# Kernel tuning notes

Hardware: AMD Instinct MI355X
Metric: run time of the kernel (lower is better)

The kernel has to match this reference:

```python
import jax, jax.numpy as jnp
import numpy as np

TEMPERATURE = 0.5
TAU_PLUS = 0.1
EPS = 1e-8


def setup_inputs() -> dict:
    key = jax.random.key(0)
    k1, k2 = jax.random.split(key)
    B, D = 8192, 128
    z_i = jax.random.normal(k1, (B, D), dtype=jnp.float32)
    z_j = jax.random.normal(k2, (B, D), dtype=jnp.float32)
    return {"z_i": z_i, "z_j": z_j}


def _l2_normalize(x, axis=1, eps=1e-12):
    # matches torch F.normalize: x / max(||x||, eps)
    n = jnp.linalg.norm(x, axis=axis, keepdims=True)
    return x / jnp.maximum(n, eps)


def reference(z_i, z_j):
    B = z_i.shape[0]
    zi = _l2_normalize(z_i, axis=1)
    zj = _l2_normalize(z_j, axis=1)
    reps = jnp.concatenate([zi, zj], axis=0)  # [2B, D]
    sim = jnp.matmul(reps, reps.T) / TEMPERATURE  # [2B, 2B]
    sim = sim - jnp.max(sim, axis=1, keepdims=True)
    mask = jnp.eye(2 * B, dtype=bool)
    sim = jnp.where(mask, -9e15, sim)
    pos = jnp.exp(jnp.sum(zi * zj, axis=-1) / TEMPERATURE)  # [B]
    positives = jnp.concatenate([pos, pos], axis=0)  # [2B]
    neg_sum = jnp.sum(jnp.exp(sim), axis=1)  # [2B]
    Ng = (-TAU_PLUS * B * positives + neg_sum) / (1.0 - TAU_PLUS)
    Ng = jnp.maximum(Ng, B * jnp.exp(jnp.asarray(-1.0 / TEMPERATURE, dtype=sim.dtype)))
    loss = -jnp.log(positives / (positives + Ng + EPS))
    return jnp.mean(loss)
```

## Files before the change

### kernel.cpp

```cpp
#include <hip/hip_runtime.h>
#include <hip/hip_bf16.h>

typedef __attribute__((ext_vector_type(8))) short bf16x8;
typedef __attribute__((ext_vector_type(4))) float f32x4;
typedef __attribute__((ext_vector_type(2))) float f32x2;

#define B_ROWS 8192
#define NROWS 16384
#define D 128
#define C1 2.8853900817779268f
#define E_M2 0.13533528323661270f
#define RSCALE 1.6986436f
#define TILE_COLS 32
#define TILE_BYTES (TILE_COLS * D * 2)
#define NSPLIT 16
#define NBLK (64 * NSPLIT)
#define NSLICE 8

__device__ __forceinline__ float fast_exp2(float x) {
#if __has_builtin(__builtin_amdgcn_exp2f)
    return __builtin_amdgcn_exp2f(x);
#else
    float r; asm("v_exp_f32 %0, %1" : "=v"(r) : "v"(x)); return r;
#endif
}
__device__ __forceinline__ float fast_log2(float x) {
#if __has_builtin(__builtin_amdgcn_logf)
    return __builtin_amdgcn_logf(x);
#else
    float r; asm("v_log_f32 %0, %1" : "=v"(r) : "v"(x)); return r;
#endif
}

__device__ __forceinline__ unsigned short f2bf(float f) {
    union { float f; unsigned u; } v; v.f = f;
    unsigned r = v.u + 0x7FFFu + ((v.u >> 16) & 1u);
    return (unsigned short)(r >> 16);
}

__device__ __host__ __forceinline__ int colpart_off(int I) {
    return I * NROWS - 128 * I * (I + 1);
}

__global__ __launch_bounds__(256) void k_norm(const float* __restrict__ zi,
                                              const float* __restrict__ zj,
                                              unsigned* __restrict__ repsU,
                                              float* __restrict__ pos) {
    int w = threadIdx.x >> 6, lane = threadIdx.x & 63;
    int row = blockIdx.x * 4 + w;
    const float2* a2 = (const float2*)(zi + (size_t)row * D);
    const float2* b2 = (const float2*)(zj + (size_t)row * D);
    float2 a = a2[lane], b = b2[lane];
    float si = a.x * a.x + a.y * a.y;
    float sj = b.x * b.x + b.y * b.y;
    float sd = a.x * b.x + a.y * b.y;
#pragma unroll
    for (int m = 32; m; m >>= 1) {
        si += __shfl_xor(si, m);
        sj += __shfl_xor(sj, m);
        sd += __shfl_xor(sd, m);
    }
    float inv_i = 1.0f / fmaxf(sqrtf(si), 1e-12f);
    float inv_j = 1.0f / fmaxf(sqrtf(sj), 1e-12f);
    float sa = inv_i * RSCALE, sb = inv_j * RSCALE;
    repsU[(size_t)row * 64 + lane] =
        (unsigned)f2bf(a.x * sa) | ((unsigned)f2bf(a.y * sa) << 16);
    repsU[(size_t)(row + B_ROWS) * 64 + lane] =
        (unsigned)f2bf(b.x * sb) | ((unsigned)f2bf(b.y * sb) << 16);
    if (lane == 0) pos[row] = fast_exp2(sd * inv_i * inv_j * C1);
}

__global__ __launch_bounds__(256, 2) void k_negsum(const unsigned short* __restrict__ R,
                                                   float* __restrict__ rowpart,
                                                   float* __restrict__ colpart) {
    __shared__ char smem[2][TILE_BYTES];
    __shared__ float colacc[2][16][16][2];
    int I = blockIdx.x >> 4;
    int s = blockIdx.x & (NSPLIT - 1);
    int rowBase = I << 8;
    int j0 = I << 3;
    int dph = (s - (j0 & 15)) & 15;
    int jstart = j0 + dph;
    int nt = (jstart < 512) ? (((511 - jstart) >> 4) + 1) : 0;

    int w = threadIdx.x >> 6;
    int lane = threadIdx.x & 63;
    int lr = lane & 15, lk = lane >> 4;
    int waveRow = rowBase + (w << 6);

    bf16x8 afrag[4][4];
#pragma unroll
    for (int r = 0; r < 4; ++r)
#pragma unroll
        for (int kk = 0; kk < 4; ++kk)
            afrag[r][kk] = *(const bf16x8*)(R + (size_t)(waveRow + r * 16 + lr) * D + kk * 32 + lk * 8);

    int srcoff[2], dstoff[2];
#pragma unroll
    for (int j = 0; j < 2; ++j) {
        int o = (w * 2 + j) * 1024 + lane * 16;
        int row = o >> 8, c = o & 255;
        srcoff[j] = row * 256 + (c ^ ((row & 7) << 4));
        dstoff[j] = (w * 2 + j) * 1024;
    }

    const char* Rb = (const char*)R;

    int m64 = (lr & 4) << 4;
    int lbase = lr * 256 + ((lk * 16) ^ ((lr & 3) << 4));

    float acc[4][4] = {};

#define STAGE(buf, jj)                                                            \
    do {                                                                          \
        const char* tb_ = Rb + (size_t)(jj) * TILE_BYTES;                         \
        _Pragma("unroll")                                                         \
        for (int j = 0; j < 2; ++j)                                               \
            __builtin_amdgcn_global_load_lds(                                     \
                (const __attribute__((address_space(1))) unsigned*)(tb_ + srcoff[j]), \
                (__attribute__((address_space(3))) unsigned*)(&smem[buf][dstoff[j]]), \
                16, 0, 0);                                                        \
    } while (0)

#define BATCH_BODY(DIAG)                                                          \
    do {                                                                          \
        _Pragma("unroll")                                                         \
        for (int ct = 0; ct < 2; ++ct) {                                          \
            const char* cb_ = sb + ct * 4096;                                     \
            bf16x8 b0 = *(const bf16x8*)(cb_ + (0 ^ m64));                        \
            bf16x8 b1 = *(const bf16x8*)(cb_ + (64 ^ m64));                       \
            bf16x8 b2 = *(const bf16x8*)(cb_ + (128 ^ m64));                      \
            bf16x8 b3 = *(const bf16x8*)(cb_ + (192 ^ m64));                      \
            _Pragma("unroll")                                                     \
            for (int r = 0; r < 4; ++r) {                                         \
                f32x4 c = {0.f, 0.f, 0.f, 0.f};                                   \
                c = __builtin_amdgcn_mfma_f32_16x16x32_bf16(afrag[r][0], b0, c, 0, 0, 0); \
                c = __builtin_amdgcn_mfma_f32_16x16x32_bf16(afrag[r][1], b1, c, 0, 0, 0); \
                c = __builtin_amdgcn_mfma_f32_16x16x32_bf16(afrag[r][2], b2, c, 0, 0, 0); \
                c = __builtin_amdgcn_mfma_f32_16x16x32_bf16(afrag[r][3], b3, c, 0, 0, 0); \
                if (DIAG && ct == r + ctd) {                                      \
                    _Pragma("unroll")                                             \
                    for (int q = 0; q < 4; ++q)                                   \
                        if (lk * 4 + q != lr) {                                   \
                            float e = fast_exp2(c[q]);                            \
                            acc[r][q] += e; csum[ct] += e;                        \
                        }                                                         \
                } else {                                                          \
                    _Pragma("unroll")                                             \
                    for (int q = 0; q < 4; ++q) {                                 \
                        float e = fast_exp2(c[q]);                                \
                        acc[r][q] += e; csum[ct] += e;                            \
                    }                                                             \
                }                                                                 \
            }                                                                     \
        }                                                                         \
    } while (0)

    if (nt > 0) STAGE(0, jstart);
    __syncthreads();
    int cur = 0;
    for (int t = 0; t < nt; ++t) {
        int jt = jstart + (t << 4);
        int colBase = jt << 5;
        if (t > 0 && w == ((t + 3) & 3) && lane < 32) {
            int pcb = colBase - 512;
            if (pcb >= rowBase + 256) {
                int par = (t - 1) & 1;
                float v = 0.f;
#pragma unroll
                for (int u = 0; u < 16; ++u) v += colacc[par][u][lane & 15][lane >> 4];
                colpart[colpart_off(I) + pcb + lane - ((I + 1) << 8)] = v;
            }
        }
        if (t + 1 < nt) STAGE(cur ^ 1, jt + 16);
        const char* sb = &smem[cur][0] + lbase;
        float csum[2] = {};
        int ctd = (waveRow - colBase) >> 4;
        bool dg = (ctd == 0) || (ctd == -2);
        if (dg) {
            BATCH_BODY(true);
        } else {
            BATCH_BODY(false);
        }
        bool offdiag = (colBase >= rowBase + 256);
        if (offdiag) {
            int par = t & 1;
            f32x2 cs = {csum[0], csum[1]};
            *(f32x2*)&colacc[par][(w << 2) | lk][lr][0] = cs;
        }
        __syncthreads();
        cur ^= 1;
    }
    if (nt > 0 && w == ((nt + 3) & 3) && lane < 32) {
        int pcb = (jstart + ((nt - 1) << 4)) << 5;
        if (pcb >= rowBase + 256) {
            int par = (nt - 1) & 1;
            float v = 0.f;
#pragma unroll
            for (int u = 0; u < 16; ++u) v += colacc[par][u][lane & 15][lane >> 4];
            colpart[colpart_off(I) + pcb + lane - ((I + 1) << 8)] = v;
        }
    }
#undef STAGE
#undef BATCH_BODY

#pragma unroll
    for (int r = 0; r < 4; ++r)
#pragma unroll
        for (int q = 0; q < 4; ++q) {
            float v = acc[r][q];
            v += __shfl_xor(v, 1);
            v += __shfl_xor(v, 2);
            v += __shfl_xor(v, 4);
            v += __shfl_xor(v, 8);
            if (lr == 0)
                rowpart[(size_t)s * NROWS + waveRow + r * 16 + lk * 4 + q] = v;
        }
}

__global__ __launch_bounds__(256) void k_negred(const float* __restrict__ rowpart,
                                                const float* __restrict__ colpart,
                                                float* __restrict__ negp) {
    int g = blockIdx.x >> 3;
    int z = blockIdx.x & (NSLICE - 1);
    int i = g * 256 + threadIdx.x;
    float a = 0.f;
#pragma unroll
    for (int s = z; s < NSPLIT; s += NSLICE)
        a += rowpart[(size_t)s * NROWS + i];
    for (int I = z; I < g; I += NSLICE)
        a += colpart[colpart_off(I) + i - ((I + 1) << 8)];
    negp[(size_t)z * NROWS + i] = a;
}

__global__ __launch_bounds__(256) void k_loss1(const float* __restrict__ pos,
                                               const float* __restrict__ negp,
                                               float* __restrict__ bsum) {
    int i = blockIdx.x * 256 + threadIdx.x;
    float neg = 0.f;
#pragma unroll
    for (int z = 0; z < NSLICE; ++z) neg += negp[(size_t)z * NROWS + i];
    neg *= E_M2;
    float p = pos[i & (B_ROWS - 1)];
    float Ng = fmaxf((neg - 819.2f * p) * (1.0f / 0.9f), 8192.0f * E_M2);
    float l = fast_log2((p + Ng + 1e-8f) / p) * 0.69314718056f;
#pragma unroll
    for (int m = 32; m; m >>= 1) l += __shfl_xor(l, m);
    __shared__ float s4[4];
    int wv = threadIdx.x >> 6;
    if ((threadIdx.x & 63) == 0) s4[wv] = l;
    __syncthreads();
    if (threadIdx.x == 0) bsum[blockIdx.x] = s4[0] + s4[1] + s4[2] + s4[3];
}

__global__ void k_loss2(const float* __restrict__ bsum, float* __restrict__ out) {
    float v = bsum[threadIdx.x];
#pragma unroll
    for (int m = 32; m; m >>= 1) v += __shfl_xor(v, m);
    if (threadIdx.x == 0) out[0] = v * (1.0f / (float)NROWS);
}

extern "C" void kernel_launch(void* const* d_in, const int* in_sizes, int n_in,
                              void* d_out, int out_size, void* d_ws, size_t ws_size,
                              hipStream_t stream) {
    const float* zi = (const float*)d_in[0];
    const float* zj = (const float*)d_in[1];
    char* ws = (char*)d_ws;
    unsigned short* reps = (unsigned short*)ws;
    float* pos = (float*)(ws + 4194304);
    float* rowpart = pos + B_ROWS;
    float* colpart = rowpart + (size_t)NSPLIT * NROWS;
    float* negp = colpart + 516096;
    float* bsum = negp + (size_t)NSLICE * NROWS;
    float* out = (float*)d_out;

    k_norm<<<B_ROWS / 4, 256, 0, stream>>>(zi, zj, (unsigned*)reps, pos);
    k_negsum<<<NBLK, 256, 0, stream>>>(reps, rowpart, colpart);
    k_negred<<<64 * NSLICE, 256, 0, stream>>>(rowpart, colpart, negp);
    k_loss1<<<NROWS / 256, 256, 0, stream>>>(pos, negp, bsum);
    k_loss2<<<1, 64, 0, stream>>>(bsum, out);
}
```

Baseline: 64.96 us.

## Software-pipeline MFMA and exp stages across column tiles

Restructures the main loop so each iteration issues the MFMAs for the current tile while running the exp/accumulate step on the previous tile's results, which are held in registers. Column-partial flushes shift one tile further back, and an epilogue drains the last tile. The goal is to let the matrix core and the transcendental/VALU work run concurrently instead of back to back. In exchange it holds 32 extra floats of accumulator state per lane, which raises register pressure and may lower occupancy.

Result: slower. 67.96 us (+4.6%).

```diff
diff --git a/kernel.cpp b/kernel.cpp
--- a/kernel.cpp
+++ b/kernel.cpp
@@ -110,6 +110,7 @@
     int lbase = lr * 256 + ((lk * 16) ^ ((lr & 3) << 4));
 
     float acc[4][4] = {};
+    f32x4 cv[2][4];
 
 #define STAGE(buf, jj)                                                            \
     do {                                                                          \
@@ -122,33 +123,46 @@
                 16, 0, 0);                                                        \
     } while (0)
 
-#define BATCH_BODY(DIAG)                                                          \
+#define MFMA_BODY(buf)                                                            \
+    do {                                                                          \
+        const char* sb = &smem[buf][0] + lbase;                                   \
+        bf16x8 bf[2][4];                                                          \
+        _Pragma("unroll")                                                         \
+        for (int ct = 0; ct < 2; ++ct)                                            \
+            _Pragma("unroll")                                                     \
+            for (int kk = 0; kk < 4; ++kk)                                        \
+                bf[ct][kk] = *(const bf16x8*)(sb + ct * 4096 + ((kk * 64) ^ m64)); \
+        _Pragma("unroll")                                                         \
+        for (int ct = 0; ct < 2; ++ct) {                                          \
+            _Pragma("unroll")                                                     \
+            for (int r = 0; r < 4; ++r) {                                         \
+                f32x4 c = {0.f, 0.f, 0.f, 0.f};                                   \
+                c = __builtin_amdgcn_mfma_f32_16x16x32_bf16(afrag[r][0], bf[ct][0], c, 0, 0, 0); \
+                c = __builtin_amdgcn_mfma_f32_16x16x32_bf16(afrag[r][1], bf[ct][1], c, 0, 0, 0); \
+                c = __builtin_amdgcn_mfma_f32_16x16x32_bf16(afrag[r][2], bf[ct][2], c, 0, 0, 0); \
+                c = __builtin_amdgcn_mfma_f32_16x16x32_bf16(afrag[r][3], bf[ct][3], c, 0, 0, 0); \
+                cv[ct][r] = c;                                                    \
+            }                                                                     \
+        }                                                                         \
+    } while (0)
+
+#define EXP_BODY(PDG)                                                             \
     do {                                                                          \
         _Pragma("unroll")                                                         \
         for (int ct = 0; ct < 2; ++ct) {                                          \
-            const char* cb_ = sb + ct * 4096;                                     \
-            bf16x8 b0 = *(const bf16x8*)(cb_ + (0 ^ m64));                        \
-            bf16x8 b1 = *(const bf16x8*)(cb_ + (64 ^ m64));                       \
-            bf16x8 b2 = *(const bf16x8*)(cb_ + (128 ^ m64));                      \
-            bf16x8 b3 = *(const bf16x8*)(cb_ + (192 ^ m64));                      \
             _Pragma("unroll")                                                     \
             for (int r = 0; r < 4; ++r) {                                         \
-                f32x4 c = {0.f, 0.f, 0.f, 0.f};                                   \
-                c = __builtin_amdgcn_mfma_f32_16x16x32_bf16(afrag[r][0], b0, c, 0, 0, 0); \
-                c = __builtin_amdgcn_mfma_f32_16x16x32_bf16(afrag[r][1], b1, c, 0, 0, 0); \
-                c = __builtin_amdgcn_mfma_f32_16x16x32_bf16(afrag[r][2], b2, c, 0, 0, 0); \
-                c = __builtin_amdgcn_mfma_f32_16x16x32_bf16(afrag[r][3], b3, c, 0, 0, 0); \
-                if (DIAG && ct == r + ctd) {                                      \
+                if (PDG && ct == r + pctd) {                                      \
                     _Pragma("unroll")                                             \
                     for (int q = 0; q < 4; ++q)                                   \
                         if (lk * 4 + q != lr) {                                   \
-                            float e = fast_exp2(c[q]);                            \
+                            float e = fast_exp2(cv[ct][r][q]);                    \
                             acc[r][q] += e; csum[ct] += e;                        \
                         }                                                         \
                 } else {                                                          \
                     _Pragma("unroll")                                             \
                     for (int q = 0; q < 4; ++q) {                                 \
-                        float e = fast_exp2(c[q]);                                \
+                        float e = fast_exp2(cv[ct][r][q]);                        \
                         acc[r][q] += e; csum[ct] += e;                            \
                     }                                                             \
                 }                                                                 \
@@ -156,53 +170,84 @@
         }                                                                         \
     } while (0)
 
-    if (nt > 0) STAGE(0, jstart);
-    __syncthreads();
-    int cur = 0;
-    for (int t = 0; t < nt; ++t) {
-        int jt = jstart + (t << 4);
-        int colBase = jt << 5;
-        if (t > 0 && w == ((t + 3) & 3) && lane < 32) {
-            int pcb = colBase - 512;
-            if (pcb >= rowBase + 256) {
-                int par = (t - 1) & 1;
-                float v = 0.f;
-#pragma unroll
-                for (int u = 0; u < 16; ++u) v += colacc[par][u][lane & 15][lane >> 4];
-                colpart[colpart_off(I) + pcb + lane - ((I + 1) << 8)] = v;
+#define FLUSH(pcb, par)                                                           \
+    do {                                                                          \
+        if ((pcb) >= rowBase + 256) {                                             \
+            float v = 0.f;                                                        \
+            _Pragma("unroll")                                                     \
+            for (int u = 0; u < 16; ++u) v += colacc[par][u][lane & 15][lane >> 4]; \
+            colpart[colpart_off(I) + (pcb) + lane - ((I + 1) << 8)] = v;          \
+        }                                                                         \
+    } while (0)
+
+    if (nt > 0) {
+        STAGE(0, jstart);
+        __syncthreads();
+        int cur = 0;
+        for (int t = 0; t < nt; ++t) {
+            int jt = jstart + (t << 4);
+            int colBase = jt << 5;
+            if (t > 1 && w == ((t + 3) & 3) && lane < 32)
+                FLUSH(colBase - 1024, (t - 2) & 1);
+            if (t + 1 < nt) STAGE(cur ^ 1, jt + 16);
+            const int pcolBase = colBase - 512;
+            {
+                const char* sb = &smem[cur][0] + lbase;
+                bf16x8 bf[2][4];
+#pragma unroll
+                for (int ct = 0; ct < 2; ++ct)
+#pragma unroll
+                    for (int kk = 0; kk < 4; ++kk)
+                        bf[ct][kk] = *(const bf16x8*)(sb + ct * 4096 + ((kk * 64) ^ m64));
+                if (t > 0) {
+                    float csum[2] = {};
+                    int pctd = (waveRow - pcolBase) >> 4;
+                    bool pdg = (pctd == 0) || (pctd == -2);
+                    if (pdg) { EXP_BODY(true); } else { EXP_BODY(false); }
+                    if (pcolBase >= rowBase + 256) {
+                        int par = (t - 1) & 1;
+                        f32x2 cs = {csum[0], csum[1]};
+                        *(f32x2*)&colacc[par][(w << 2) | lk][lr][0] = cs;
+                    }
+                }
+#pragma unroll
+                for (int ct = 0; ct < 2; ++ct) {
+#pragma unroll
+                    for (int r = 0; r < 4; ++r) {
+                        f32x4 c = {0.f, 0.f, 0.f, 0.f};
+                        c = __builtin_amdgcn_mfma_f32_16x16x32_bf16(afrag[r][0], bf[ct][0], c, 0, 0, 0);
+                        c = __builtin_amdgcn_mfma_f32_16x16x32_bf16(afrag[r][1], bf[ct][1], c, 0, 0, 0);
+                        c = __builtin_amdgcn_mfma_f32_16x16x32_bf16(afrag[r][2], bf[ct][2], c, 0, 0, 0);
+                        c = __builtin_amdgcn_mfma_f32_16x16x32_bf16(afrag[r][3], bf[ct][3], c, 0, 0, 0);
+                        cv[ct][r] = c;
+                    }
+                }
+            }
+            __syncthreads();
+            cur ^= 1;
+        }
+        {
+            const int pcolBase = (jstart + ((nt - 1) << 4)) << 5;
+            float csum[2] = {};
+            int pctd = (waveRow - pcolBase) >> 4;
+            bool pdg = (pctd == 0) || (pctd == -2);
+            if (pdg) { EXP_BODY(true); } else { EXP_BODY(false); }
+            if (pcolBase >= rowBase + 256) {
+                int par = (nt - 1) & 1;
+                f32x2 cs = {csum[0], csum[1]};
+                *(f32x2*)&colacc[par][(w << 2) | lk][lr][0] = cs;
             }
         }
-        if (t + 1 < nt) STAGE(cur ^ 1, jt + 16);
-        const char* sb = &smem[cur][0] + lbase;
-        float csum[2] = {};
-        int ctd = (waveRow - colBase) >> 4;
-        bool dg = (ctd == 0) || (ctd == -2);
-        if (dg) {
-            BATCH_BODY(true);
-        } else {
-            BATCH_BODY(false);
-        }
-        bool offdiag = (colBase >= rowBase + 256);
-        if (offdiag) {
-            int par = t & 1;
-            f32x2 cs = {csum[0], csum[1]};
-            *(f32x2*)&colacc[par][(w << 2) | lk][lr][0] = cs;
-        }
         __syncthreads();
-        cur ^= 1;
-    }
-    if (nt > 0 && w == ((nt + 3) & 3) && lane < 32) {
-        int pcb = (jstart + ((nt - 1) << 4)) << 5;
-        if (pcb >= rowBase + 256) {
-            int par = (nt - 1) & 1;
-            float v = 0.f;
-#pragma unroll
-            for (int u = 0; u < 16; ++u) v += colacc[par][u][lane & 15][lane >> 4];
-            colpart[colpart_off(I) + pcb + lane - ((I + 1) << 8)] = v;
-        }
+        if (nt >= 2 && w == 0 && lane < 32)
+            FLUSH((jstart + ((nt - 2) << 4)) << 5, (nt - 2) & 1);
+        if (w == 1 && lane < 32)
+            FLUSH((jstart + ((nt - 1) << 4)) << 5, (nt - 1) & 1);
     }
 #undef STAGE
-#undef BATCH_BODY
+#undef MFMA_BODY
+#undef EXP_BODY
+#undef FLUSH
 
 #pragma unroll
     for (int r = 0; r < 4; ++r)
```
